# Kernel tuning notes

Measured on AMD Instinct MI355X. Metric: run time of the kernel, lower is better.

Reference implementation:

```python
import jax, jax.numpy as jnp
import numpy as np

NEG_INF = -1e30  # stand-in for -inf that is safe under fp16/bf16


def setup_inputs() -> dict:
    key = jax.random.key(0)
    k1, k2, k3, k4, k5 = jax.random.split(key, 5)
    B, NC, H, Wd = 32, 256, 64, 64
    MW, E = 32, 768
    images = jax.random.normal(k1, (B, NC, H, Wd), dtype=jnp.float32)
    words = jax.random.normal(k2, (B, MW, E), dtype=jnp.float32)
    # mask: True where word is ignored; ensure at least one word is attended per row
    mask = jax.random.randint(k3, (B, MW), 0, 2).astype(bool)
    mask = mask.at[:, 0].set(False)
    W = jax.random.normal(k4, (NC, E), dtype=jnp.float32) * (1.0 / np.sqrt(E))
    b = jax.random.normal(k5, (NC,), dtype=jnp.float32) * 0.01
    return {"images": images, "words": words, "mask": mask, "W": W, "b": b}


def reference(images, words, mask, W, b):
    B, NC, H, Wd = images.shape
    _, MW, E = words.shape
    # 1x1 conv over words == linear projection emb_dim -> nc_in
    # words_p: [B, nc_in, max_words]
    words_p = jnp.einsum('bme,ce->bcm', words, W) + b[None, :, None]
    # images flattened to pixels: [B, h*w, nc_in]
    imgs = images.reshape(B, NC, H * Wd).transpose(0, 2, 1)
    # attention scores: [B, h*w, max_words], scaled by 1/sqrt(nc_in)
    attn = jnp.einsum('bpc,bcm->bpm', imgs, words_p) * (1.0 / np.sqrt(NC))
    attn = jnp.where(mask[:, None, :], NEG_INF, attn)
    attn = jax.nn.softmax(attn, axis=-1)
    # weighted word sum per pixel: [B, nc_in, h*w]
    weighted = jnp.einsum('bcm,bpm->bcp', words_p, attn)
    weighted_words = weighted.reshape(B, NC, H, Wd)
    attn_out = attn.transpose(0, 2, 1).reshape(B, MW, H, Wd)
    return weighted_words, attn_out
```

## Files before the change

### kernel.cpp

```cpp
#include <hip/hip_runtime.h>
#include <math.h>

#define B_   32
#define NC_  256
#define HW_  4096
#define MW_  32
#define E_   768
#define NEG_BIG -3.0e38f

#define PART_OFF   0
#define WP_OFF     2097152
#define WT_OFF     2359296
#define WORDST_OFF 2555904
#define MASK_OFF   3342336

__global__ __launch_bounds__(256) void prep_kernel(
    const float* __restrict__ W, const float* __restrict__ words,
    const void* __restrict__ mask_raw,
    float* __restrict__ WT, float* __restrict__ wordsT,
    int* __restrict__ maskn) {
  const int tid = threadIdx.x;
  const int tx = tid & 31, ty = tid >> 5;
  if (blockIdx.x < 192) {
    __shared__ float t[32][33];
    const int tc = blockIdx.x / 24, te = blockIdx.x % 24;
    const int c0 = tc * 32, e0 = te * 32;
#pragma unroll
    for (int k = 0; k < 4; ++k) {
      const int r = ty + 8 * k;
      t[r][tx] = W[(c0 + r) * E_ + e0 + tx];
    }
    __syncthreads();
#pragma unroll
    for (int k = 0; k < 4; ++k) {
      const int r = ty + 8 * k;
      WT[(e0 + r) * NC_ + c0 + tx] = t[tx][r];
    }
  } else if (blockIdx.x < 960) {
    __shared__ float t[32][33];
    const int idx = blockIdx.x - 192;
    const int b = idx / 24, te = idx % 24;
    const int e0 = te * 32;
    const float* wsrc = words + (size_t)b * MW_ * E_;
    float* wdst = wordsT + (size_t)b * E_ * MW_;
#pragma unroll
    for (int k = 0; k < 4; ++k) {
      const int m = ty + 8 * k;
      t[m][tx] = wsrc[m * E_ + e0 + tx];
    }
    __syncthreads();
#pragma unroll
    for (int k = 0; k < 4; ++k) {
      const int e = ty + 8 * k;
      wdst[(e0 + e) * MW_ + tx] = t[tx][e];
    }
  } else {
    __shared__ int is_word;
    if (tid == 0) is_word = 1;
    __syncthreads();
    const int* mi = (const int*)mask_raw;
    const int v = mi[tid];
    if (v != 0 && v != 1 && v != 0x3F800000) is_word = 0;
    __syncthreads();
    if (is_word) {
#pragma unroll
      for (int j = 0; j < 4; ++j) { const int i = j * 256 + tid; maskn[i] = (mi[i] != 0); }
    } else {
      const unsigned char* mb = (const unsigned char*)mask_raw;
#pragma unroll
      for (int j = 0; j < 4; ++j) { const int i = j * 256 + tid; maskn[i] = (mb[i] != 0); }
    }
  }
}

__global__ __launch_bounds__(256) void stage1_partial(
    const float* __restrict__ wordsT, const float* __restrict__ WT,
    float* __restrict__ part) {
  const int c = threadIdx.x;
  const int b = blockIdx.x >> 3;
  const int chunk = blockIdx.x & 7;
  const int e0 = chunk * 96;
  const float* wt = wordsT + (size_t)b * E_ * MW_;
  float acc[32];
#pragma unroll
  for (int m = 0; m < 32; ++m) acc[m] = 0.f;
#pragma unroll 2
  for (int e = e0; e < e0 + 96; ++e) {
    const float wv = WT[(size_t)e * NC_ + c];
    const float* wr = wt + e * MW_;
#pragma unroll
    for (int m = 0; m < 32; ++m) acc[m] = fmaf(wv, wr[m], acc[m]);
  }
  float* pp = part + ((size_t)chunk * 32 + b) * 32 * 256;
#pragma unroll
  for (int m = 0; m < 32; ++m) pp[m * 256 + c] = acc[m];
}

__global__ __launch_bounds__(256) void stage1_reduce(
    const float* __restrict__ part, const float* __restrict__ bias,
    float* __restrict__ wp) {
  const int idx = blockIdx.x * 256 + threadIdx.x;
  const int c = idx & 255;
  const int m = (idx >> 8) & 31;
  const int b = idx >> 13;
  float s = bias[c];
#pragma unroll
  for (int k = 0; k < 8; ++k)
    s += part[(((size_t)k * 32 + b) * 32 + m) * 256 + c];
  wp[((size_t)b * 256 + c) * 32 + m] = s;
}

__global__ __launch_bounds__(256) void attention_main(
    const float* __restrict__ images, const float* __restrict__ wp,
    const int* __restrict__ maskn, float* __restrict__ out_w,
    float* __restrict__ out_a) {
  const int b = blockIdx.x >> 4;
  const int p = ((blockIdx.x & 15) << 8) + threadIdx.x;
  const float* img = images + (size_t)b * NC_ * HW_ + p;
  const float* wpb = wp + (size_t)b * NC_ * MW_;

  float s[32];
#pragma unroll
  for (int m = 0; m < 32; ++m) s[m] = 0.f;

  float cur[16];
#pragma unroll
  for (int j = 0; j < 16; ++j)
    cur[j] = __builtin_nontemporal_load(img + ((size_t)j << 12));

#pragma unroll 1
  for (int c0 = 0; c0 < 256; c0 += 16) {
    float nxt[16];
    if (c0 + 16 < 256) {
#pragma unroll
      for (int j = 0; j < 16; ++j)
        nxt[j] = __builtin_nontemporal_load(img + ((size_t)(c0 + 16 + j) << 12));
    }
#pragma unroll
    for (int j = 0; j < 16; ++j) {
#pragma unroll
      for (int m = 0; m < 32; ++m)
        s[m] = fmaf(cur[j], wpb[((c0 + j) << 5) + m], s[m]);
    }
#pragma unroll
    for (int j = 0; j < 16; ++j) cur[j] = nxt[j];
  }

  unsigned mbits = 0;
#pragma unroll
  for (int m = 0; m < 32; ++m)
    mbits |= (maskn[(b << 5) + m] != 0 ? 1u : 0u) << m;

  float mx = NEG_BIG;
#pragma unroll
  for (int m = 0; m < 32; ++m) {
    s[m] *= 0.0625f;
    if (!((mbits >> m) & 1u)) mx = fmaxf(mx, s[m]);
  }
  float sum = 0.f;
#pragma unroll
  for (int m = 0; m < 32; ++m) {
    const float ev = ((mbits >> m) & 1u) ? 0.f : __expf(s[m] - mx);
    s[m] = ev;
    sum += ev;
  }
  const float inv = 1.f / sum;
#pragma unroll
  for (int m = 0; m < 32; ++m) {
    const float a = s[m] * inv;
    s[m] = a;
    __builtin_nontemporal_store(a, out_a + ((size_t)(b * 32 + m) << 12) + p);
  }

#pragma unroll 1
  for (int c0 = 0; c0 < 256; c0 += 8) {
#pragma unroll
    for (int jc = 0; jc < 8; ++jc) {
      const int c = c0 + jc;
      float o = 0.f;
#pragma unroll
      for (int m = 0; m < 32; ++m)
        o = fmaf(wpb[(c << 5) + m], s[m], o);
      __builtin_nontemporal_store(o, out_w + ((size_t)(b * 256 + c) << 12) + p);
    }
  }
}

extern "C" void kernel_launch(void* const* d_in, const int* in_sizes, int n_in,
                              void* d_out, int out_size, void* d_ws, size_t ws_size,
                              hipStream_t stream) {
  const float* images = (const float*)d_in[0];
  const float* words  = (const float*)d_in[1];
  const void*  mask   = d_in[2];
  const float* W      = (const float*)d_in[3];
  const float* bias   = (const float*)d_in[4];

  float* ws     = (float*)d_ws;
  float* part   = ws + PART_OFF;
  float* wp     = ws + WP_OFF;
  float* WT     = ws + WT_OFF;
  float* wordsT = ws + WORDST_OFF;
  int*   maskn  = (int*)(ws + MASK_OFF);

  float* out_w = (float*)d_out;
  float* out_a = out_w + (size_t)B_ * NC_ * HW_;

  prep_kernel<<<961, 256, 0, stream>>>(W, words, mask, WT, wordsT, maskn);
  stage1_partial<<<256, 256, 0, stream>>>(wordsT, WT, part);
  stage1_reduce<<<1024, 256, 0, stream>>>(part, bias, wp);
  attention_main<<<512, 256, 0, stream>>>(images, wp, maskn, out_w, out_a);
}
```

Measured before the change: 336.0 us.

## Split channel reduction across four waves per block with shared-memory combine

Each block now covers 64 pixels instead of 256, and its four wavefronts each reduce a quarter of the channels. The partial scores are combined through shared memory, and then each wave writes a quarter of the attention maps and of the weighted-word outputs. This launches 2048 blocks instead of 512 to raise parallelism and occupancy and to shorten the serial per-thread loops on a memory-bound kernel. In exchange it adds a shared-memory reduction, a barrier, and redundant softmax work in every wave, and it drops the explicit software prefetch of image rows.

```diff
diff --git a/kernel.cpp b/kernel.cpp
--- a/kernel.cpp
+++ b/kernel.cpp
@@ -110,41 +110,43 @@
   wp[((size_t)b * 256 + c) * 32 + m] = s;
 }
 
-__global__ __launch_bounds__(256) void attention_main(
+__global__ __launch_bounds__(256) void attention_fused(
     const float* __restrict__ images, const float* __restrict__ wp,
     const int* __restrict__ maskn, float* __restrict__ out_w,
     float* __restrict__ out_a) {
-  const int b = blockIdx.x >> 4;
-  const int p = ((blockIdx.x & 15) << 8) + threadIdx.x;
-  const float* img = images + (size_t)b * NC_ * HW_ + p;
+  __shared__ float part[4][32][64];
+  const int b = blockIdx.x >> 6;
+  const int p0 = (blockIdx.x & 63) << 6;
+  const int wv = threadIdx.x >> 6;
+  const int ln = threadIdx.x & 63;
+  const int p = p0 + ln;
+  const float* img = images + ((size_t)(b * NC_ + (wv << 6))) * HW_ + p;
   const float* wpb = wp + (size_t)b * NC_ * MW_;
 
   float s[32];
 #pragma unroll
   for (int m = 0; m < 32; ++m) s[m] = 0.f;
-
-  float cur[16];
-#pragma unroll
-  for (int j = 0; j < 16; ++j)
-    cur[j] = __builtin_nontemporal_load(img + ((size_t)j << 12));
-
 #pragma unroll 1
-  for (int c0 = 0; c0 < 256; c0 += 16) {
-    float nxt[16];
-    if (c0 + 16 < 256) {
-#pragma unroll
-      for (int j = 0; j < 16; ++j)
-        nxt[j] = __builtin_nontemporal_load(img + ((size_t)(c0 + 16 + j) << 12));
-    }
-#pragma unroll
-    for (int j = 0; j < 16; ++j) {
+  for (int cc = 0; cc < 64; cc += 8) {
+    float cur[8];
+#pragma unroll
+    for (int j = 0; j < 8; ++j)
+      cur[j] = __builtin_nontemporal_load(img + (size_t)(cc + j) * HW_);
+#pragma unroll
+    for (int j = 0; j < 8; ++j) {
+      const int c = (wv << 6) + cc + j;
 #pragma unroll
       for (int m = 0; m < 32; ++m)
-        s[m] = fmaf(cur[j], wpb[((c0 + j) << 5) + m], s[m]);
-    }
-#pragma unroll
-    for (int j = 0; j < 16; ++j) cur[j] = nxt[j];
-  }
+        s[m] = fmaf(cur[j], wpb[(c << 5) + m], s[m]);
+    }
+  }
+#pragma unroll
+  for (int m = 0; m < 32; ++m) part[wv][m][ln] = s[m];
+  __syncthreads();
+
+#pragma unroll
+  for (int m = 0; m < 32; ++m)
+    s[m] = (part[0][m][ln] + part[1][m][ln]) + (part[2][m][ln] + part[3][m][ln]);
 
   unsigned mbits = 0;
 #pragma unroll
@@ -167,22 +169,19 @@
   const float inv = 1.f / sum;
 #pragma unroll
   for (int m = 0; m < 32; ++m) {
-    const float a = s[m] * inv;
-    s[m] = a;
-    __builtin_nontemporal_store(a, out_a + ((size_t)(b * 32 + m) << 12) + p);
-  }
-
-#pragma unroll 1
-  for (int c0 = 0; c0 < 256; c0 += 8) {
-#pragma unroll
-    for (int jc = 0; jc < 8; ++jc) {
-      const int c = c0 + jc;
-      float o = 0.f;
-#pragma unroll
-      for (int m = 0; m < 32; ++m)
-        o = fmaf(wpb[(c << 5) + m], s[m], o);
-      __builtin_nontemporal_store(o, out_w + ((size_t)(b * 256 + c) << 12) + p);
-    }
+    s[m] *= inv;
+    if ((m >> 3) == wv)
+      __builtin_nontemporal_store(s[m], out_a + ((size_t)(b * 32 + m) << 12) + p);
+  }
+
+#pragma unroll 2
+  for (int i = 0; i < 64; ++i) {
+    const int c = (wv << 6) + i;
+    float o = 0.f;
+#pragma unroll
+    for (int m = 0; m < 32; ++m)
+      o = fmaf(wpb[(c << 5) + m], s[m], o);
+    __builtin_nontemporal_store(o, out_w + ((size_t)(b * 256 + c) << 12) + p);
   }
 }
 
@@ -208,5 +207,5 @@
   prep_kernel<<<961, 256, 0, stream>>>(W, words, mask, WT, wordsT, maskn);
   stage1_partial<<<256, 256, 0, stream>>>(wordsT, WT, part);
   stage1_reduce<<<1024, 256, 0, stream>>>(part, bias, wp);
-  attention_main<<<512, 256, 0, stream>>>(images, wp, maskn, out_w, out_a);
-}
+  attention_fused<<<2048, 256, 0, stream>>>(images, wp, maskn, out_w, out_a);
+}
```

Measured after the change: 505.2 us. +50.4%, slower.
